# Optimization experiments

Measured on AMD Instinct MI355X. Metric: run time of the kernel, lower is better.

## Reference

```python
import jax, jax.numpy as jnp
import numpy as np

N_RAYS = 16384
PTS_PER_RAY = 256
M = N_RAYS * PTS_PER_RAY
ALPHA_INIT = 0.01


def setup_inputs() -> dict:
    key = jax.random.key(0)
    k1, k2 = jax.random.split(key)
    density = jax.random.normal(k1, (M,), dtype=jnp.float32)
    ray_id = jnp.sort(jax.random.randint(k2, (M,), 0, N_RAYS)).astype(jnp.int32)
    shift = jnp.full((1,), np.log(1.0 / (1.0 - ALPHA_INIT) - 1.0), dtype=jnp.float32)
    interval = jnp.full((1,), 0.5, dtype=jnp.float32)
    return {"density": density, "ray_id": ray_id, "shift": shift, "interval": interval, "N": N_RAYS}


def reference(density, ray_id, shift, interval, N):
    # Raw2Alpha: alpha = 1 - exp(-softplus(density + shift) * interval)
    #           => log(1 - alpha) = -softplus(density + shift) * interval (exact, stable)
    sp = jax.nn.softplus(density + shift[0])            # [M]
    log_one_minus_alpha = -sp * interval[0]             # [M], <= 0
    alpha = -jnp.expm1(log_one_minus_alpha)             # [M]

    # Alphas2Weights: per-ray exclusive cumprod of (1-alpha) in log space.
    cs = jnp.cumsum(log_one_minus_alpha)                # inclusive global cumsum
    ex = cs - log_one_minus_alpha                       # exclusive global cumsum (non-increasing)
    # value of ex at the first element of each ray = segment max (ex is non-increasing)
    base = jax.ops.segment_max(ex, ray_id, num_segments=N)  # [N]
    T = jnp.exp(ex - base[ray_id])                      # exclusive per-ray transmittance
    weights = T * alpha                                 # [M]
    # alphainv_last = prod(1-alpha) over each ray (empty rays -> 1)
    log_total = jax.ops.segment_sum(log_one_minus_alpha, ray_id, num_segments=N)
    alphainv_last = jnp.exp(log_total)                  # [N]
    return weights, alphainv_last
```

## Files before the change

### kernel.cpp

```cpp
#include <hip/hip_runtime.h>
#include <hip/hip_bf16.h>


__global__ void VoxelNeRF_find_starts(const int* __restrict__ ray_id,
                                      int* __restrict__ start,
                                      int M, int N) {
    int i = blockIdx.x * blockDim.x + threadIdx.x;
    if (i >= M) return;
    int cur  = ray_id[i];
    int prev = (i == 0) ? -1 : ray_id[i - 1];
    for (int r = prev + 1; r <= cur; ++r) start[r] = i;
    if (i == M - 1) {
        for (int r = cur + 1; r <= N; ++r) start[r] = M;
    }
}

__global__ __launch_bounds__(256) void VoxelNeRF_scan(
    const float* __restrict__ density,
    const int*   __restrict__ start,
    const float* __restrict__ shift_p,
    const float* __restrict__ interval_p,
    float* __restrict__ weights,
    float* __restrict__ alphainv_last,
    int N) {
    const int wave = threadIdx.x >> 6;
    const int lane = threadIdx.x & 63;
    const int r = blockIdx.x * 4 + wave;
    if (r >= N) return;

    const int s = start[r];
    const int e = start[r + 1];
    const float shift    = shift_p[0];
    const float interval = interval_p[0];

    float carry = 0.0f;

    for (int base = s; base < e; base += 64) {
        const int i = base + lane;
        float lom = 0.0f;
        float alpha = 0.0f;
        if (i < e) {
            const float x  = density[i] + shift;
            const float sp = fmaxf(x, 0.0f) + log1pf(expf(-fabsf(x)));
            lom   = -sp * interval;
            alpha = -expm1f(lom);
        }
        float v = lom;
        #pragma unroll
        for (int off = 1; off < 64; off <<= 1) {
            float t = __shfl_up(v, off, 64);
            if (lane >= off) v += t;
        }
        const float ex = carry + (v - lom);
        if (i < e) {
            weights[i] = expf(ex) * alpha;
        }
        carry += __shfl(v, 63, 64);
    }

    if (lane == 0) {
        alphainv_last[r] = expf(carry);
    }
}

extern "C" void kernel_launch(void* const* d_in, const int* in_sizes, int n_in,
                              void* d_out, int out_size, void* d_ws, size_t ws_size,
                              hipStream_t stream) {
    const float* density    = (const float*)d_in[0];
    const int*   ray_id     = (const int*)d_in[1];
    const float* shift_p    = (const float*)d_in[2];
    const float* interval_p = (const float*)d_in[3];
    const int M = in_sizes[0];
    const int N = out_size - M;

    float* weights       = (float*)d_out;
    float* alphainv_last = (float*)d_out + M;
    int*   start         = (int*)d_ws;

    {
        const int threads = 256;
        const int blocks  = (M + threads - 1) / threads;
        VoxelNeRF_find_starts<<<blocks, threads, 0, stream>>>(ray_id, start, M, N);
    }
    {
        const int waves_per_block = 4;
        const int blocks = (N + waves_per_block - 1) / waves_per_block;
        VoxelNeRF_scan<<<blocks, 256, 0, stream>>>(
            density, start, shift_p, interval_p, weights, alphainv_last, N);
    }
}
```

Before: 107.8 us.

## Process six elements per lane with DPP wave scan and fast math

The per-ray scan now has each lane handle six consecutive elements, scanning them serially, then does one DPP-based inclusive wave scan over the lane sums instead of a shuffle-based scan per 64 elements. It swaps precise exp/log1p/expm1 for __expf/__logf intrinsics and uses readlane for the carry. The find_starts kernel loads four ray ids per thread with an int4 load. The goal is fewer cross-lane operations and less transcendental cost per element. In exchange, per-lane strided access is less coalesced, the int4 load assumes M is a multiple of four, and the fast intrinsics reduce accuracy.

```diff
diff --git a/kernel.cpp b/kernel.cpp
--- a/kernel.cpp
+++ b/kernel.cpp
@@ -2,16 +2,39 @@
 #include <hip/hip_bf16.h>
 
 
+#define ELEMS_PER_LANE 6
+#define CHUNK (64 * ELEMS_PER_LANE)
+
+__device__ __forceinline__ float wave_incl_scan(float x) {
+    float v = x;
+    v += __int_as_float(__builtin_amdgcn_update_dpp(0, __float_as_int(v), 0x111, 0xf, 0xf, true));
+    v += __int_as_float(__builtin_amdgcn_update_dpp(0, __float_as_int(v), 0x112, 0xf, 0xf, true));
+    v += __int_as_float(__builtin_amdgcn_update_dpp(0, __float_as_int(v), 0x114, 0xf, 0xf, true));
+    v += __int_as_float(__builtin_amdgcn_update_dpp(0, __float_as_int(v), 0x118, 0xf, 0xf, true));
+    v += __int_as_float(__builtin_amdgcn_update_dpp(0, __float_as_int(v), 0x142, 0xa, 0xf, false));
+    v += __int_as_float(__builtin_amdgcn_update_dpp(0, __float_as_int(v), 0x143, 0xc, 0xf, false));
+    return v;
+}
+
 __global__ void VoxelNeRF_find_starts(const int* __restrict__ ray_id,
                                       int* __restrict__ start,
                                       int M, int N) {
-    int i = blockIdx.x * blockDim.x + threadIdx.x;
-    if (i >= M) return;
-    int cur  = ray_id[i];
-    int prev = (i == 0) ? -1 : ray_id[i - 1];
-    for (int r = prev + 1; r <= cur; ++r) start[r] = i;
-    if (i == M - 1) {
-        for (int r = cur + 1; r <= N; ++r) start[r] = M;
+    const int j  = blockIdx.x * blockDim.x + threadIdx.x;
+    const int i0 = j * 4;
+    if (i0 >= M) return;
+    const int4 v = *reinterpret_cast<const int4*>(ray_id + i0);
+    int prev = (i0 == 0) ? -1 : ray_id[i0 - 1];
+    const int ids0 = v.x, ids1 = v.y, ids2 = v.z, ids3 = v.w;
+    #pragma unroll
+    for (int k = 0; k < 4; ++k) {
+        const int cur = (k == 0) ? ids0 : (k == 1) ? ids1 : (k == 2) ? ids2 : ids3;
+        if (cur != prev) {
+            for (int r = prev + 1; r <= cur; ++r) start[r] = i0 + k;
+        }
+        prev = cur;
+    }
+    if (i0 + 4 >= M) {
+        for (int r = prev + 1; r <= N; ++r) start[r] = M;
     }
 }
 
@@ -35,31 +58,46 @@
 
     float carry = 0.0f;
 
-    for (int base = s; base < e; base += 64) {
-        const int i = base + lane;
-        float lom = 0.0f;
-        float alpha = 0.0f;
-        if (i < e) {
-            const float x  = density[i] + shift;
-            const float sp = fmaxf(x, 0.0f) + log1pf(expf(-fabsf(x)));
-            lom   = -sp * interval;
-            alpha = -expm1f(lom);
+    for (int base = s; base < e; base += CHUNK) {
+        const int i0 = base + lane * ELEMS_PER_LANE;
+
+        float lm[ELEMS_PER_LANE];
+        float al[ELEMS_PER_LANE];
+        float pk[ELEMS_PER_LANE];
+        float lane_sum = 0.0f;
+
+        #pragma unroll
+        for (int k = 0; k < ELEMS_PER_LANE; ++k) {
+            const int i = i0 + k;
+            float lomk = 0.0f, alk = 0.0f;
+            if (i < e) {
+                const float x  = density[i] + shift;
+                const float sp = fmaxf(x, 0.0f) + __logf(1.0f + __expf(-fabsf(x)));
+                lomk = -sp * interval;
+                alk  = 1.0f - __expf(lomk);
+            }
+            lm[k] = lomk;
+            al[k] = alk;
+            pk[k] = lane_sum;
+            lane_sum += lomk;
         }
-        float v = lom;
+
+        const float v_incl = wave_incl_scan(lane_sum);
+        const float excl_lane = carry + (v_incl - lane_sum);
+
         #pragma unroll
-        for (int off = 1; off < 64; off <<= 1) {
-            float t = __shfl_up(v, off, 64);
-            if (lane >= off) v += t;
+        for (int k = 0; k < ELEMS_PER_LANE; ++k) {
+            const int i = i0 + k;
+            if (i < e) {
+                weights[i] = __expf(excl_lane + pk[k]) * al[k];
+            }
         }
-        const float ex = carry + (v - lom);
-        if (i < e) {
-            weights[i] = expf(ex) * alpha;
-        }
-        carry += __shfl(v, 63, 64);
+
+        carry += __int_as_float(__builtin_amdgcn_readlane(__float_as_int(v_incl), 63));
     }
 
     if (lane == 0) {
-        alphainv_last[r] = expf(carry);
+        alphainv_last[r] = __expf(carry);
     }
 }
 
@@ -79,7 +117,8 @@
 
     {
         const int threads = 256;
-        const int blocks  = (M + threads - 1) / threads;
+        const int elems   = (M + 3) / 4;
+        const int blocks  = (elems + threads - 1) / threads;
         VoxelNeRF_find_starts<<<blocks, threads, 0, stream>>>(ray_id, start, M, N);
     }
     {
```

Result: faster. 95.54 us (-11.3%).
